# Performance work log

Measured on AMD Instinct MI355X. Metric: run time of the kernel, lower is better.

The kernel has to match this reference:

```python
import jax, jax.numpy as jnp
import numpy as np
import math

N = 20000          # real nodes (batch_size)
D = 256            # hidden_dim
H = 4              # num_heads
L = 3              # num_layers
E = 320000         # local edges
EXP_DEG = 4        # expander_degree
LN_EPS = 1e-5


def setup_inputs() -> dict:
    key = jax.random.key(0)
    ks = jax.random.split(key, 8)
    x = jax.random.normal(ks[0], (N, D), jnp.float32)
    rng = np.random.default_rng(0)
    edge_index = jnp.asarray(rng.integers(0, N, size=(2, E)), dtype=jnp.int32)
    # Expander: EXP_DEG//2 random permutations on N+1 nodes (incl. virtual node),
    # each contributing edges in both directions -> degree-EXP_DEG regular graph.
    n = N + 1
    perms = [rng.permutation(n) for _ in range(EXP_DEG // 2)]
    src = np.concatenate([np.arange(n) for _ in perms] + perms)
    dst = np.concatenate(perms + [np.arange(n) for _ in perms])
    exp_edge_index = jnp.asarray(np.stack([src, dst]), dtype=jnp.int32)
    s_in = 1.0 / math.sqrt(D)
    s_ffn = 1.0 / math.sqrt(4 * D)
    def w(k, shape, s):
        return jax.random.normal(k, shape, jnp.float32) * s
    params = {
        'Wqkv_loc': w(ks[1], (L, D, 3 * D), s_in), 'bqkv_loc': jnp.zeros((L, 3 * D), jnp.float32),
        'Wo_loc':   w(ks[2], (L, D, D), s_in),     'bo_loc':   jnp.zeros((L, D), jnp.float32),
        'Wqkv_exp': w(ks[3], (L, D, 3 * D), s_in), 'bqkv_exp': jnp.zeros((L, 3 * D), jnp.float32),
        'Wo_exp':   w(ks[4], (L, D, D), s_in),     'bo_exp':   jnp.zeros((L, D), jnp.float32),
        'ln_g': jnp.ones((L, D), jnp.float32),     'ln_b': jnp.zeros((L, D), jnp.float32),
        'W1': w(ks[5], (L, D, 4 * D), s_in),       'b1': jnp.zeros((L, 4 * D), jnp.float32),
        'W2': w(ks[6], (L, 4 * D, D), s_ffn),      'b2': jnp.zeros((L, D), jnp.float32),
    }
    return {'x': x, 'edge_index': edge_index, 'exp_edge_index': exp_edge_index, **params}


def _attention(h, src, dst, Wqkv, bqkv, Wo, bo):
    # Sparse multi-head attention over (src -> dst) edges with segment softmax per dst.
    n, d = h.shape
    dh = d // H
    qkv = (h @ Wqkv + bqkv).reshape(n, 3, H, dh)
    q, k, v = qkv[:, 0], qkv[:, 1], qkv[:, 2]            # [n, H, dh]
    score = (q[dst] * k[src]).sum(-1) / jnp.sqrt(jnp.float32(dh))  # [e, H]
    m = jax.ops.segment_max(score, dst, num_segments=n)  # [n, H]
    ex = jnp.exp(score - m[dst])
    denom = jax.ops.segment_sum(ex, dst, num_segments=n)
    alpha = ex / (denom[dst] + 1e-16)
    out = jax.ops.segment_sum(alpha[:, :, None] * v[src], dst, num_segments=n)  # [n, H, dh]
    return out.reshape(n, d) @ Wo + bo


def _layer_norm(x, g, b):
    mu = x.mean(-1, keepdims=True)
    var = ((x - mu) ** 2).mean(-1, keepdims=True)
    return (x - mu) * jax.lax.rsqrt(var + LN_EPS) * g + b


def reference(x, edge_index, exp_edge_index, Wqkv_loc, bqkv_loc, Wo_loc, bo_loc,
              Wqkv_exp, bqkv_exp, Wo_exp, bo_exp, ln_g, ln_b, W1, b1, W2, b2):
    n0 = x.shape[0]
    # VirtualNode transform: append one zero-feature node connected to/from all nodes.
    h = jnp.concatenate([x, jnp.zeros((1, x.shape[1]), x.dtype)], axis=0)
    ar = jnp.arange(n0, dtype=edge_index.dtype)
    vn = jnp.full((n0,), n0, dtype=edge_index.dtype)
    src = jnp.concatenate([edge_index[0], ar, vn])
    dst = jnp.concatenate([edge_index[1], vn, ar])
    esrc, edst = exp_edge_index[0], exp_edge_index[1]
    for l in range(L):  # fixed small number of structurally distinct layers
        res = h
        loc = _attention(h, src, dst, Wqkv_loc[l], bqkv_loc[l], Wo_loc[l], bo_loc[l])
        exp = _attention(h, esrc, edst, Wqkv_exp[l], bqkv_exp[l], Wo_exp[l], bo_exp[l])
        h = _layer_norm(res + loc + exp, ln_g[l], ln_b[l])
        h = h + (jax.nn.gelu(h @ W1[l] + b1[l], approximate=False) @ W2[l] + b2[l])
    return h[:n0]
```

## Files before the change

kernel.cpp:

```cpp
#include <hip/hip_runtime.h>
#include <stdint.h>

#define NREAL   20000
#define NNODES  20001
#define VN      20000
#define E_EDGES 320000
#define NEXP    80004
#define MPAD    20096
#define NVNW    320

typedef unsigned short u16;
typedef unsigned int   u32;
typedef __bf16 bf16x8 __attribute__((ext_vector_type(8)));
typedef float  f32x4  __attribute__((ext_vector_type(4)));

__device__ __host__ __forceinline__ size_t fmoff(int row, int col, int LD) {
    return (size_t)(row >> 4) * ((size_t)LD * 16) + (size_t)((col >> 3) * 128)
         + (size_t)((row & 15) * 8) + (size_t)(col & 7);
}

__device__ __forceinline__ float bf2f(u16 v) {
    union { u32 u; float f; } x; x.u = ((u32)v) << 16; return x.f;
}
__device__ __forceinline__ u16 f2bf(float f) {
    union { float f; u32 u; } x; x.f = f;
    u32 r = (x.u + 0x7fffu + ((x.u >> 16) & 1u)) >> 16;
    return (u16)r;
}
__device__ __forceinline__ float4 cvt4(ushort4 u) {
    return make_float4(bf2f(u.x), bf2f(u.y), bf2f(u.z), bf2f(u.w));
}
__device__ __forceinline__ float4 ld4bf(const u16* p) { return cvt4(*(const ushort4*)p); }


__global__ void hinit_kernel(const float* __restrict__ x, float* __restrict__ h,
                             u16* __restrict__ hb) {
    int idx = blockIdx.x * 256 + threadIdx.x;
    if (idx >= NNODES * 64) return;
    int row = idx >> 6, c0 = (idx & 63) * 4;
    float4 v = make_float4(0.f, 0.f, 0.f, 0.f);
    if (row < NREAL) v = *(const float4*)(x + (size_t)row * 256 + c0);
    *(float4*)(h + (size_t)row * 256 + c0) = v;
    ushort4 o;
    o.x = f2bf(v.x); o.y = f2bf(v.y); o.z = f2bf(v.z); o.w = f2bf(v.w);
    *(ushort4*)(hb + fmoff(row, c0, 256)) = o;
}

__global__ void init_kernel(int* cnt, int* fill, int* ecnt,
                            const float* __restrict__ bl, const float* __restrict__ be,
                            float* __restrict__ bcat,
                            const float* __restrict__ bol, const float* __restrict__ boe,
                            float* __restrict__ bsum) {
    int i = blockIdx.x * 256 + threadIdx.x;
    if (i < NREAL) { cnt[i] = 0; fill[i] = 0; }
    if (i < NNODES) ecnt[i] = 0;
    if (i < 3 * 1536) {
        int l = i / 1536, c = i - l * 1536;
        bcat[i] = (c < 768) ? bl[l * 768 + c] : be[l * 768 + c - 768];
    }
    if (i < 3 * 256) bsum[i] = bol[i] + boe[i];
}

__global__ void csr_count_kernel(const int* __restrict__ ei, int* __restrict__ cnt) {
    int e = blockIdx.x * 256 + threadIdx.x;
    if (e < E_EDGES) atomicAdd(&cnt[ei[E_EDGES + e]], 1);
}

__global__ void csr_scan_kernel(const int* __restrict__ cnt, int* __restrict__ indptr) {
    __shared__ int ssum[256];
    int t = threadIdx.x;
    int c0 = t * 79;
    int s = 0;
    for (int j = 0; j < 79; j++) {
        int i = c0 + j;
        if (i < NREAL) s += cnt[i];
    }
    ssum[t] = s;
    __syncthreads();
    for (int d2 = 1; d2 < 256; d2 <<= 1) {
        int v = (t >= d2) ? ssum[t - d2] : 0;
        __syncthreads();
        ssum[t] += v;
        __syncthreads();
    }
    int run = (t == 0) ? 0 : ssum[t - 1];
    for (int j = 0; j < 79; j++) {
        int i = c0 + j;
        if (i < NREAL) { indptr[i] = run; run += cnt[i]; }
    }
    if (t == 255) indptr[NREAL] = run;
}

__global__ void csr_scatter_kernel(const int* __restrict__ ei, const int* __restrict__ indptr,
                                   int* __restrict__ fill, int* __restrict__ srcs) {
    int e = blockIdx.x * 256 + threadIdx.x;
    if (e < E_EDGES) {
        int d = ei[E_EDGES + e];
        int pos = indptr[d] + atomicAdd(&fill[d], 1);
        srcs[pos] = ei[e];
    }
}

__global__ void exp_scatter_kernel(const int* __restrict__ eei, int* __restrict__ ecnt,
                                   int* __restrict__ esrcs) {
    int e = blockIdx.x * 256 + threadIdx.x;
    if (e < NEXP) {
        int d = eei[NEXP + e];
        int pos = atomicAdd(&ecnt[d], 1);
        esrcs[d * 4 + pos] = eei[e];
    }
}

__global__ void wconv_all_kernel(const float* __restrict__ WqkvL, const float* __restrict__ WqkvE,
                                 const float* __restrict__ WoL, const float* __restrict__ WoE,
                                 const float* __restrict__ W1, const float* __restrict__ W2,
                                 u16* __restrict__ out) {
    int i = blockIdx.x * 256 + threadIdx.x;
    if (i >= 3 * 1048576) return;
    int l = i / 1048576, r = i - l * 1048576;
    if (r >= 393216 && r < 524288) {
        int r2 = r - 393216;
        int k = r2 >> 8, n = r2 & 255;
        float v = (k < 256) ? WoL[(size_t)l * 65536 + k * 256 + n]
                            : WoE[(size_t)l * 65536 + (k - 256) * 256 + n];
        out[(size_t)l * 1048576 + 393216 + fmoff(n, k, 512)] = f2bf(v);
        return;
    }
    const float* src; int K, N; int base;
    if (r < 196608)      { src = WqkvL; K = 256;  N = 768;  base = 0; }
    else if (r < 393216) { src = WqkvE; K = 256;  N = 768;  base = 196608; }
    else if (r < 786432) { src = W1;    K = 256;  N = 1024; base = 524288; }
    else                 { src = W2;    K = 1024; N = 256;  base = 786432; }
    int r2 = r - base;
    int k = r2 / N, n = r2 - k * N;
    out[(size_t)l * 1048576 + base + fmoff(n, k, K)] = f2bf(src[(size_t)l * K * N + r2]);
}

template <int EPI>
__global__ __launch_bounds__(256) void gemm_bn(
    const u16* __restrict__ A, const u16* __restrict__ Bt, const float* __restrict__ bias,
    u16* Cb, u16* Q0, u16* KV0, u16* Q1, u16* KV1, int M, int Nout, int nbn) {
    __shared__ u16 lB[128 * 256];
    const int lin = blockIdx.x;
    const int xcd = lin & 7, rest = lin >> 3;
    const int nt = rest % nbn, mc = xcd + 8 * (rest / nbn);
    const int tn = nt * 128;
    const int tid = threadIdx.x;
    const int w = tid >> 6, lane = tid & 63;
    const int lm = lane & 15, q = lane >> 4;

    {
        const u16* bsrc = Bt + (size_t)(tn >> 4) * 4096;
#pragma unroll
        for (int r = 0; r < 16; r++) {
            int o = (r * 256 + tid) * 8;
            *(bf16x8*)&lB[o] = *(const bf16x8*)&bsrc[o];
        }
    }
    __syncthreads();

    f32x4 acc[2][8];
#pragma unroll
    for (int a = 0; a < 2; a++)
#pragma unroll
        for (int b = 0; b < 8; b++) acc[a][b] = (f32x4)0.0f;

    const int lbo = q * 128 + lm * 8;
    const int maxp = MPAD / 16 - 1;

    bf16x8 aS[3][2], bS[2][8];
#pragma unroll
    for (int s = 0; s < 2; s++) {
        int p0 = (mc * 4) * 8 + w * 2;
#pragma unroll
        for (int f = 0; f < 2; f++) {
            int p = p0 + f; if (p > maxp) p = maxp;
            aS[s][f] = *(const bf16x8*)(A + (size_t)p * 4096 + s * 512 + lbo);
        }
#pragma unroll
        for (int n = 0; n < 8; n++)
            bS[s][n] = *(const bf16x8*)&lB[n * 4096 + s * 512 + lbo];
    }

#pragma unroll
    for (int t = 0; t < 32; t++) {
        const int mt = t >> 3, kk = t & 7;
        if (t + 2 < 32) {
            const int t2 = t + 2, mt2 = t2 >> 3, kk2 = t2 & 7;
            int p0 = (mc * 4 + mt2) * 8 + w * 2;
#pragma unroll
            for (int f = 0; f < 2; f++) {
                int p = p0 + f; if (p > maxp) p = maxp;
                aS[t2 % 3][f] = *(const bf16x8*)(A + (size_t)p * 4096 + kk2 * 512 + lbo);
            }
        }
        if (t >= 1 && t + 1 < 32) {
            const int kk1 = (t + 1) & 7;
#pragma unroll
            for (int n = 0; n < 8; n++)
                bS[(t + 1) & 1][n] = *(const bf16x8*)&lB[n * 4096 + kk1 * 512 + lbo];
        }
#pragma unroll
        for (int mi = 0; mi < 2; mi++)
#pragma unroll
            for (int ni = 0; ni < 8; ni++)
                acc[mi][ni] = __builtin_amdgcn_mfma_f32_16x16x32_bf16(
                    bS[t & 1][ni], aS[t % 3][mi], acc[mi][ni], 0, 0, 0);

        if (kk == 7) {
            const int tmg = (mc * 4 + mt) * 128;
#pragma unroll
            for (int mi = 0; mi < 2; mi++) {
                int grow = tmg + w * 32 + mi * 16 + lm;
                if (grow < M) {
#pragma unroll
                    for (int ni = 0; ni < 8; ni++) {
                        int gcol = tn + ni * 16 + q * 4;
                        float4 b4 = *(const float4*)(bias + gcol);
                        float v0 = acc[mi][ni][0] + b4.x;
                        float v1 = acc[mi][ni][1] + b4.y;
                        float v2 = acc[mi][ni][2] + b4.z;
                        float v3 = acc[mi][ni][3] + b4.w;
                        if constexpr (EPI == 6) {
                            ushort4 o;
                            o.x = f2bf(v0); o.y = f2bf(v1); o.z = f2bf(v2); o.w = f2bf(v3);
                            u16* dst;
                            if (gcol < 256)       dst = Q0  + (size_t)grow * 256 + gcol;
                            else if (gcol < 768)  dst = KV0 + (size_t)grow * 512 + (gcol - 256);
                            else if (gcol < 1024) dst = Q1  + (size_t)grow * 256 + (gcol - 768);
                            else                  dst = KV1 + (size_t)grow * 512 + (gcol - 1024);
                            *(ushort4*)dst = o;
                        } else {
                            float g0, g1, g2, g3;
                            {
                                float u = 0.7978845608f * (v0 + 0.044715f * v0 * v0 * v0);
                                g0 = 0.5f * v0 * (2.0f - 2.0f / (__expf(2.0f * u) + 1.0f));
                            }
                            {
                                float u = 0.7978845608f * (v1 + 0.044715f * v1 * v1 * v1);
                                g1 = 0.5f * v1 * (2.0f - 2.0f / (__expf(2.0f * u) + 1.0f));
                            }
                            {
                                float u = 0.7978845608f * (v2 + 0.044715f * v2 * v2 * v2);
                                g2 = 0.5f * v2 * (2.0f - 2.0f / (__expf(2.0f * u) + 1.0f));
                            }
                            {
                                float u = 0.7978845608f * (v3 + 0.044715f * v3 * v3 * v3);
                                g3 = 0.5f * v3 * (2.0f - 2.0f / (__expf(2.0f * u) + 1.0f));
                            }
                            ushort4 o;
                            o.x = f2bf(g0); o.y = f2bf(g1); o.z = f2bf(g2); o.w = f2bf(g3);
                            *(ushort4*)(Cb + fmoff(grow, gcol, Nout)) = o;
                        }
                    }
                }
#pragma unroll
                for (int ni = 0; ni < 8; ni++) acc[mi][ni] = (f32x4)0.0f;
            }
        }
    }
}

template <int EPI, int K, int MT>
__global__ __launch_bounds__(256) void gemm_fm(
    const u16* __restrict__ A, const u16* __restrict__ Bt, const float* __restrict__ bias,
    u16* Cb, float* Cf, const float* resid, int M, int Nout, int nby) {
    constexpr int MFR = MT / 32;
    constexpr int NK = K / 32;
    const int lin = blockIdx.x;
    const int xcd = lin & 7, sub = lin >> 3;
    const int mtile = xcd + 8 * (sub / nby);
    const int ntile = sub - (sub / nby) * nby;
    const int tm = mtile * MT, tn = ntile * 128;
    if (tm >= M) return;

    const int tid = threadIdx.x;
    const int w = tid >> 6, lane = tid & 63;
    const int lm = lane & 15, q = lane >> 4;
    const int mo = (w >> 1) * (MT / 2), no = (w & 1) * 64;

    f32x4 acc[MFR][4];
#pragma unroll
    for (int a = 0; a < MFR; a++)
#pragma unroll
        for (int b = 0; b < 4; b++) acc[a][b] = (f32x4)0.0f;

    const u16* apf[MFR];
    const u16* bpf[4];
#pragma unroll
    for (int t = 0; t < MFR; t++) {
        int p = (tm + mo) / 16 + t;
        apf[t] = A + (size_t)p * (16 * K) + q * 128 + lm * 8;
    }
#pragma unroll
    for (int n = 0; n < 4; n++) {
        int c = (tn + no) / 16 + n;
        bpf[n] = Bt + (size_t)c * (16 * K) + q * 128 + lm * 8;
    }

    bf16x8 sA[3][MFR], sB[3][4];
#pragma unroll
    for (int s = 0; s < 2 && s < NK; s++) {
#pragma unroll
        for (int t = 0; t < MFR; t++) sA[s][t] = *(const bf16x8*)(apf[t] + s * 512);
#pragma unroll
        for (int n = 0; n < 4; n++) sB[s][n] = *(const bf16x8*)(bpf[n] + s * 512);
    }
#pragma unroll
    for (int i = 0; i < NK; i++) {
        const int cu = i % 3, pf = (i + 2) % 3;
        if (i + 2 < NK) {
#pragma unroll
            for (int t = 0; t < MFR; t++) sA[pf][t] = *(const bf16x8*)(apf[t] + (i + 2) * 512);
#pragma unroll
            for (int n = 0; n < 4; n++) sB[pf][n] = *(const bf16x8*)(bpf[n] + (i + 2) * 512);
        }
#pragma unroll
        for (int mi = 0; mi < MFR; mi++)
#pragma unroll
            for (int ni = 0; ni < 4; ni++)
                acc[mi][ni] = __builtin_amdgcn_mfma_f32_16x16x32_bf16(
                    sB[cu][ni], sA[cu][mi], acc[mi][ni], 0, 0, 0);
    }

    float4 b4[4];
#pragma unroll
    for (int ni = 0; ni < 4; ni++)
        b4[ni] = *(const float4*)(bias + tn + no + ni * 16 + q * 4);

#pragma unroll
    for (int mi = 0; mi < MFR; mi++) {
        int grow = tm + mo + mi * 16 + lm;
        if constexpr (EPI == 4) { if (grow >= NREAL) continue; }
        else                    { if (grow >= M) continue; }
#pragma unroll
        for (int ni = 0; ni < 4; ni++) {
            int gcol = tn + no + ni * 16 + q * 4;
            float v0 = acc[mi][ni][0] + b4[ni].x;
            float v1 = acc[mi][ni][1] + b4[ni].y;
            float v2 = acc[mi][ni][2] + b4[ni].z;
            float v3 = acc[mi][ni][3] + b4[ni].w;
            size_t idx = (size_t)grow * Nout + gcol;
            if constexpr (EPI == 1) {
                *(float4*)(Cf + idx) = make_float4(v0, v1, v2, v3);
            } else if constexpr (EPI == 3) {
                float4 rv = *(const float4*)(resid + idx);
                float o0 = rv.x + v0, o1 = rv.y + v1, o2 = rv.z + v2, o3 = rv.w + v3;
                *(float4*)(Cf + idx) = make_float4(o0, o1, o2, o3);
                ushort4 o;
                o.x = f2bf(o0); o.y = f2bf(o1); o.z = f2bf(o2); o.w = f2bf(o3);
                *(ushort4*)(Cb + fmoff(grow, gcol, Nout)) = o;
            } else {
                float4 rv = *(const float4*)(resid + idx);
                *(float4*)(Cf + idx) = make_float4(rv.x + v0, rv.y + v1, rv.z + v2, rv.w + v3);
            }
        }
    }
}

__global__ void vn_online_kernel(const u16* __restrict__ qb, const u16* __restrict__ kv,
                                 float* __restrict__ part) {
    int lane = threadIdx.x & 63;
    int h = lane >> 4;
    int off = (h << 6) + (lane & 15) * 4;
    float4 qv = ld4bf(qb + (size_t)VN * 256 + off);
    int wv = (int)((blockIdx.x * (size_t)blockDim.x + threadIdx.x) >> 6);
    float m = -1e30f, l = 0.0f;
    float ax = 0, ay = 0, az = 0, aw = 0;
    for (int i = wv; i < NREAL; i += NVNW) {
        const u16* p = kv + (size_t)i * 512 + off;
        float4 k4 = ld4bf(p);
        float4 v4 = ld4bf(p + 256);
        float s = qv.x * k4.x + qv.y * k4.y + qv.z * k4.z + qv.w * k4.w;
        s += __shfl_xor(s, 1); s += __shfl_xor(s, 2);
        s += __shfl_xor(s, 4); s += __shfl_xor(s, 8);
        float sc = s * 0.125f;
        float mn = fmaxf(m, sc);
        float fold = __expf(m - mn);
        float ee = __expf(sc - mn);
        ax = ax * fold + v4.x * ee;
        ay = ay * fold + v4.y * ee;
        az = az * fold + v4.z * ee;
        aw = aw * fold + v4.w * ee;
        l = l * fold + ee;
        m = mn;
    }
    float* pp = part + (size_t)wv * 264;
    if ((lane & 15) == 0) { pp[h] = m; pp[4 + h] = l; }
    *(float4*)(pp + 8 + off) = make_float4(ax, ay, az, aw);
}

__global__ void vn_merge_kernel(const float* __restrict__ part, u16* __restrict__ acat) {
    __shared__ float sm[4][64][6];
    int w = threadIdx.x >> 6, lane = threadIdx.x & 63;
    int h = lane >> 4;
    int off = (h << 6) + (lane & 15) * 4;
    float M = -1e30f, L = 0.0f;
    float ax = 0, ay = 0, az = 0, aw = 0;
    for (int p = w * 80; p < w * 80 + 80; p++) {
        const float* pp = part + (size_t)p * 264;
        float pm = pp[h], pl = pp[4 + h];
        float4 nm = *(const float4*)(pp + 8 + off);
        float Mn = fmaxf(M, pm);
        float s0 = __expf(M - Mn);
        float s1 = __expf(pm - Mn);
        ax = ax * s0 + nm.x * s1;
        ay = ay * s0 + nm.y * s1;
        az = az * s0 + nm.z * s1;
        aw = aw * s0 + nm.w * s1;
        L = L * s0 + pl * s1;
        M = Mn;
    }
    sm[w][lane][0] = M; sm[w][lane][1] = L;
    sm[w][lane][2] = ax; sm[w][lane][3] = ay;
    sm[w][lane][4] = az; sm[w][lane][5] = aw;
    __syncthreads();
    if (w == 0) {
        float M2 = -1e30f, L2 = 0.0f;
        float bx = 0, by = 0, bz = 0, bw = 0;
#pragma unroll
        for (int p = 0; p < 4; p++) {
            float pm = sm[p][lane][0], pl = sm[p][lane][1];
            float Mn = fmaxf(M2, pm);
            float s0 = __expf(M2 - Mn);
            float s1 = __expf(pm - Mn);
            bx = bx * s0 + sm[p][lane][2] * s1;
            by = by * s0 + sm[p][lane][3] * s1;
            bz = bz * s0 + sm[p][lane][4] * s1;
            bw = bw * s0 + sm[p][lane][5] * s1;
            L2 = L2 * s0 + pl * s1;
            M2 = Mn;
        }
        float inv = 1.0f / (L2 + 1e-16f);
        ushort4 o;
        o.x = f2bf(bx * inv); o.y = f2bf(by * inv);
        o.z = f2bf(bz * inv); o.w = f2bf(bw * inv);
        *(ushort4*)(acat + fmoff(VN, off, 512)) = o;
    }
}

__global__ void attn_fused_kernel(const u16* __restrict__ qb_loc, const u16* __restrict__ kv_loc,
                                  const u16* __restrict__ qb_exp, const u16* __restrict__ kv_exp,
                                  const int* __restrict__ indptr, const int* __restrict__ srcs,
                                  const int* __restrict__ esrcs,
                                  u16* __restrict__ acat) {
    int gw = (int)((blockIdx.x * (size_t)blockDim.x + threadIdx.x) >> 6);
    int lane = threadIdx.x & 63;
    int off = ((lane >> 4) << 6) + (lane & 15) * 4;

    const u16 *qb, *kv;
    const int* sl;
    int node, beg, deg, tot, cbase;
    if (gw < NREAL) {
        node = gw; qb = qb_loc; kv = kv_loc; sl = srcs; cbase = 0;
        beg = indptr[node]; deg = indptr[node + 1] - beg; tot = deg + 1;
    } else if (gw < NREAL + NNODES) {
        node = gw - NREAL;
        qb = qb_exp; kv = kv_exp; sl = esrcs; cbase = 256;
        beg = node * 4; deg = 4; tot = 4;
    } else {
        return;
    }

    float4 qv = ld4bf(qb + (size_t)node * 256 + off);
    float m = -1e30f, l = 0.0f;
    float ax = 0, ay = 0, az = 0, aw = 0;

    if (tot <= 4) {
        ushort4 kraw[4], vraw[4];
#pragma unroll
        for (int j = 0; j < 4; j++) {
            int s = (j < deg) ? sl[beg + j] : VN;
            const u16* p = kv + (size_t)s * 512 + off;
            kraw[j] = *(const ushort4*)p;
            vraw[j] = *(const ushort4*)(p + 256);
        }
        float sc[4];
#pragma unroll
        for (int j = 0; j < 4; j++) {
            float4 k4 = cvt4(kraw[j]);
            float p = qv.x * k4.x + qv.y * k4.y + qv.z * k4.z + qv.w * k4.w;
            p += __shfl_xor(p, 1); p += __shfl_xor(p, 2);
            p += __shfl_xor(p, 4); p += __shfl_xor(p, 8);
            sc[j] = (j < tot) ? p * 0.125f : -1e30f;
        }
        float mn = fmaxf(fmaxf(sc[0], sc[1]), fmaxf(sc[2], sc[3]));
#pragma unroll
        for (int j = 0; j < 4; j++) {
            float ee = __expf(sc[j] - mn);
            float4 v4 = cvt4(vraw[j]);
            ax += v4.x * ee; ay += v4.y * ee; az += v4.z * ee; aw += v4.w * ee;
            l += ee;
        }
        m = mn;
    } else {
        for (int e0 = 0; e0 < tot; e0 += 8) {
            ushort4 kraw[8], vraw[8];
#pragma unroll
            for (int j = 0; j < 8; j++) {
                int e = e0 + j;
                int s = (e < deg) ? sl[beg + e] : VN;
                const u16* p = kv + (size_t)s * 512 + off;
                kraw[j] = *(const ushort4*)p;
                vraw[j] = *(const ushort4*)(p + 256);
            }
            float sc[8];
#pragma unroll
            for (int j = 0; j < 8; j++) {
                float4 k4 = cvt4(kraw[j]);
                float p = qv.x * k4.x + qv.y * k4.y + qv.z * k4.z + qv.w * k4.w;
                p += __shfl_xor(p, 1); p += __shfl_xor(p, 2);
                p += __shfl_xor(p, 4); p += __shfl_xor(p, 8);
                sc[j] = (e0 + j < tot) ? p * 0.125f : -1e30f;
            }
            float cmax = fmaxf(fmaxf(fmaxf(sc[0], sc[1]), fmaxf(sc[2], sc[3])),
                               fmaxf(fmaxf(sc[4], sc[5]), fmaxf(sc[6], sc[7])));
            float mn = fmaxf(m, cmax);
            float fold = __expf(m - mn);
            ax *= fold; ay *= fold; az *= fold; aw *= fold; l *= fold;
#pragma unroll
            for (int j = 0; j < 8; j++) {
                float ee = __expf(sc[j] - mn);
                float4 v4 = cvt4(vraw[j]);
                ax += v4.x * ee; ay += v4.y * ee; az += v4.z * ee; aw += v4.w * ee;
                l += ee;
            }
            m = mn;
        }
    }
    float inv = 1.0f / (l + 1e-16f);
    ushort4 o;
    o.x = f2bf(ax * inv); o.y = f2bf(ay * inv);
    o.z = f2bf(az * inv); o.w = f2bf(aw * inv);
    *(ushort4*)(acat + fmoff(node, cbase + off, 512)) = o;
}

__global__ void ln_kernel(const float* hin, const float* __restrict__ asum,
                          const float* __restrict__ g, const float* __restrict__ b,
                          float* hout, u16* __restrict__ hb) {
    int row = blockIdx.x * 4 + (threadIdx.x >> 6);
    if (row >= NNODES) return;
    int lane = threadIdx.x & 63;
    size_t base = (size_t)row * 256 + lane * 4;
    float4 xv = *(const float4*)(hin + base);
    float4 av = *(const float4*)(asum + base);
    xv.x += av.x; xv.y += av.y; xv.z += av.z; xv.w += av.w;
    float s = xv.x + xv.y + xv.z + xv.w;
#pragma unroll
    for (int o = 1; o < 64; o <<= 1) s += __shfl_xor(s, o);
    float mu = s * (1.0f / 256.0f);
    float dx = xv.x - mu, dy = xv.y - mu, dz = xv.z - mu, dw = xv.w - mu;
    float ss = dx * dx + dy * dy + dz * dz + dw * dw;
#pragma unroll
    for (int o = 1; o < 64; o <<= 1) ss += __shfl_xor(ss, o);
    float var = ss * (1.0f / 256.0f);
    float inv = 1.0f / sqrtf(var + 1e-5f);
    float4 gv = *(const float4*)(g + lane * 4);
    float4 bv = *(const float4*)(b + lane * 4);
    float4 y;
    y.x = dx * inv * gv.x + bv.x;
    y.y = dy * inv * gv.y + bv.y;
    y.z = dz * inv * gv.z + bv.z;
    y.w = dw * inv * gv.w + bv.w;
    *(float4*)(hout + base) = y;
    ushort4 o4;
    o4.x = f2bf(y.x); o4.y = f2bf(y.y); o4.z = f2bf(y.z); o4.w = f2bf(y.w);
    *(ushort4*)(hb + fmoff(row, lane * 4, 256)) = o4;
}


extern "C" void kernel_launch(void* const* d_in, const int* in_sizes, int n_in,
                              void* d_out, int out_size, void* d_ws, size_t ws_size,
                              hipStream_t stream) {
    (void)in_sizes; (void)n_in; (void)out_size; (void)ws_size;
    const float* x        = (const float*)d_in[0];
    const int*   ei       = (const int*)d_in[1];
    const int*   eei      = (const int*)d_in[2];
    const float* Wqkv_loc = (const float*)d_in[3];
    const float* bqkv_loc = (const float*)d_in[4];
    const float* Wo_loc   = (const float*)d_in[5];
    const float* bo_loc   = (const float*)d_in[6];
    const float* Wqkv_exp = (const float*)d_in[7];
    const float* bqkv_exp = (const float*)d_in[8];
    const float* Wo_exp   = (const float*)d_in[9];
    const float* bo_exp   = (const float*)d_in[10];
    const float* ln_g     = (const float*)d_in[11];
    const float* ln_b     = (const float*)d_in[12];
    const float* W1       = (const float*)d_in[13];
    const float* b1       = (const float*)d_in[14];
    const float* W2       = (const float*)d_in[15];
    const float* b2       = (const float*)d_in[16];

    char* wsp = (char*)d_ws;
    size_t off = 0;
    auto carve = [&](size_t bytes) -> void* {
        void* p = wsp + off;
        off += (bytes + 255) & ~(size_t)255;
        return p;
    };
    float* h_f    = (float*)carve((size_t)NNODES * 256 * 4);
    u16*   h_b    = (u16*)carve((size_t)MPAD * 256 * 2);
    u16*   qb_loc = (u16*)carve((size_t)NNODES * 256 * 2);
    u16*   kv_loc = (u16*)carve((size_t)NNODES * 512 * 2);
    u16*   qb_exp = (u16*)carve((size_t)NNODES * 256 * 2);
    u16*   kv_exp = (u16*)carve((size_t)NNODES * 512 * 2);
    u16*   acat   = (u16*)carve((size_t)MPAD * 512 * 2);
    float* asum   = (float*)carve((size_t)NNODES * 256 * 4);
    u16*   wbf    = (u16*)carve((size_t)3 * 1048576 * 2);
    float* bcat   = (float*)carve((size_t)3 * 1536 * 4);
    float* bsum   = (float*)carve((size_t)3 * 256 * 4);
    int*   cnt    = (int*)carve((size_t)NREAL * 4);
    int*   indptr = (int*)carve((size_t)(NREAL + 1) * 4);
    int*   fill   = (int*)carve((size_t)NREAL * 4);
    int*   srcs   = (int*)carve((size_t)E_EDGES * 4);
    int*   ecnt   = (int*)carve((size_t)NNODES * 4);
    int*   esrcs  = (int*)carve((size_t)NNODES * 4 * 4);
    float* part   = (float*)carve((size_t)NVNW * 264 * 4);
    u16*   mid    = qb_loc;

    hinit_kernel<<<(NNODES * 64 + 255) / 256, 256, 0, stream>>>(x, h_f, h_b);
    init_kernel<<<(NNODES + 255) / 256, 256, 0, stream>>>(
        cnt, fill, ecnt, bqkv_loc, bqkv_exp, bcat, bo_loc, bo_exp, bsum);
    csr_count_kernel<<<(E_EDGES + 255) / 256, 256, 0, stream>>>(ei, cnt);
    csr_scan_kernel<<<1, 256, 0, stream>>>(cnt, indptr);
    csr_scatter_kernel<<<(E_EDGES + 255) / 256, 256, 0, stream>>>(ei, indptr, fill, srcs);
    exp_scatter_kernel<<<(NEXP + 255) / 256, 256, 0, stream>>>(eei, ecnt, esrcs);
    wconv_all_kernel<<<(3 * 1048576 + 255) / 256, 256, 0, stream>>>(
        Wqkv_loc, Wqkv_exp, Wo_loc, Wo_exp, W1, W2, wbf);

    const int NBM64 = 320;

    for (int l = 0; l < 3; l++) {
        const u16* wqkvC = wbf + (size_t)l * 1048576 + 0;
        const u16* wocat = wbf + (size_t)l * 1048576 + 393216;
        const u16* w1T   = wbf + (size_t)l * 1048576 + 524288;
        const u16* w2T   = wbf + (size_t)l * 1048576 + 786432;

        gemm_bn<6><<<480, 256, 0, stream>>>(
            h_b, wqkvC, bcat + l * 1536, nullptr,
            qb_loc, kv_loc, qb_exp, kv_exp, NNODES, 1536, 12);

        vn_online_kernel<<<NVNW / 4, 256, 0, stream>>>(qb_loc, kv_loc, part);
        vn_merge_kernel<<<1, 256, 0, stream>>>(part, acat);

        attn_fused_kernel<<<10001, 256, 0, stream>>>(
            qb_loc, kv_loc, qb_exp, kv_exp, indptr, srcs, esrcs, acat);

        gemm_fm<1, 512, 64><<<NBM64 * 2, 256, 0, stream>>>(
            acat, wocat, bsum + l * 256, nullptr, asum, nullptr, NNODES, 256, 2);

        ln_kernel<<<(NNODES + 3) / 4, 256, 0, stream>>>(
            h_f, asum, ln_g + l * 256, ln_b + l * 256, h_f, h_b);

        gemm_bn<2><<<320, 256, 0, stream>>>(
            h_b, w1T, b1 + l * 1024, mid,
            nullptr, nullptr, nullptr, nullptr, NNODES, 1024, 8);
        if (l < 2) {
            gemm_fm<3, 1024, 64><<<NBM64 * 2, 256, 0, stream>>>(
                mid, w2T, b2 + l * 256, h_b, h_f, h_f, NNODES, 256, 2);
        } else {
            gemm_fm<4, 1024, 64><<<NBM64 * 2, 256, 0, stream>>>(
                mid, w2T, b2 + l * 256, nullptr, (float*)d_out, h_f, NNODES, 256, 2);
        }
    }
}
```

Before: 910.5 us.

## Interleave K/V per lane, fuse VN attention into edge kernel, prefetch gathers

The QKV GEMM epilogue now stores K and V interleaved, so each lane fetches its 4 K and 4 V values with a single 16-byte load instead of two 8-byte loads in both attention paths. The virtual-node online-softmax kernel is folded into the fused edge-attention kernel as extra leading warps, which removes one launch and lets that work overlap with the per-node attention. The high-degree path also double-buffers the gathers for the next 8 edges while computing the current chunk. The cost is more registers in the prefetch path, which may lower occupancy, and the VN warps are now scheduled alongside the edge warps.

```diff
diff --git a/kernel.cpp b/kernel.cpp
--- a/kernel.cpp
+++ b/kernel.cpp
@@ -13,6 +13,7 @@
 typedef unsigned int   u32;
 typedef __bf16 bf16x8 __attribute__((ext_vector_type(8)));
 typedef float  f32x4  __attribute__((ext_vector_type(4)));
+typedef u16    u16x8  __attribute__((ext_vector_type(8)));
 
 __device__ __host__ __forceinline__ size_t fmoff(int row, int col, int LD) {
     return (size_t)(row >> 4) * ((size_t)LD * 16) + (size_t)((col >> 3) * 128)
@@ -31,6 +32,12 @@
     return make_float4(bf2f(u.x), bf2f(u.y), bf2f(u.z), bf2f(u.w));
 }
 __device__ __forceinline__ float4 ld4bf(const u16* p) { return cvt4(*(const ushort4*)p); }
+__device__ __forceinline__ float4 cvtk8(u16x8 r) {
+    return make_float4(bf2f(r[0]), bf2f(r[1]), bf2f(r[2]), bf2f(r[3]));
+}
+__device__ __forceinline__ float4 cvtv8(u16x8 r) {
+    return make_float4(bf2f(r[4]), bf2f(r[5]), bf2f(r[6]), bf2f(r[7]));
+}
 
 
 __global__ void hinit_kernel(const float* __restrict__ x, float* __restrict__ h,
@@ -225,10 +232,17 @@
                             ushort4 o;
                             o.x = f2bf(v0); o.y = f2bf(v1); o.z = f2bf(v2); o.w = f2bf(v3);
                             u16* dst;
-                            if (gcol < 256)       dst = Q0  + (size_t)grow * 256 + gcol;
-                            else if (gcol < 768)  dst = KV0 + (size_t)grow * 512 + (gcol - 256);
-                            else if (gcol < 1024) dst = Q1  + (size_t)grow * 256 + (gcol - 768);
-                            else                  dst = KV1 + (size_t)grow * 512 + (gcol - 1024);
+                            if (gcol < 256) {
+                                dst = Q0 + (size_t)grow * 256 + gcol;
+                            } else if (gcol < 768) {
+                                int c = gcol - 256;
+                                dst = KV0 + (size_t)grow * 512 + ((c & 255) >> 2) * 8 + ((c >> 8) << 2);
+                            } else if (gcol < 1024) {
+                                dst = Q1 + (size_t)grow * 256 + (gcol - 768);
+                            } else {
+                                int c = gcol - 1024;
+                                dst = KV1 + (size_t)grow * 512 + ((c & 255) >> 2) * 8 + ((c >> 8) << 2);
+                            }
                             *(ushort4*)dst = o;
                         } else {
                             float g0, g1, g2, g3;
@@ -358,38 +372,6 @@
     }
 }
 
-__global__ void vn_online_kernel(const u16* __restrict__ qb, const u16* __restrict__ kv,
-                                 float* __restrict__ part) {
-    int lane = threadIdx.x & 63;
-    int h = lane >> 4;
-    int off = (h << 6) + (lane & 15) * 4;
-    float4 qv = ld4bf(qb + (size_t)VN * 256 + off);
-    int wv = (int)((blockIdx.x * (size_t)blockDim.x + threadIdx.x) >> 6);
-    float m = -1e30f, l = 0.0f;
-    float ax = 0, ay = 0, az = 0, aw = 0;
-    for (int i = wv; i < NREAL; i += NVNW) {
-        const u16* p = kv + (size_t)i * 512 + off;
-        float4 k4 = ld4bf(p);
-        float4 v4 = ld4bf(p + 256);
-        float s = qv.x * k4.x + qv.y * k4.y + qv.z * k4.z + qv.w * k4.w;
-        s += __shfl_xor(s, 1); s += __shfl_xor(s, 2);
-        s += __shfl_xor(s, 4); s += __shfl_xor(s, 8);
-        float sc = s * 0.125f;
-        float mn = fmaxf(m, sc);
-        float fold = __expf(m - mn);
-        float ee = __expf(sc - mn);
-        ax = ax * fold + v4.x * ee;
-        ay = ay * fold + v4.y * ee;
-        az = az * fold + v4.z * ee;
-        aw = aw * fold + v4.w * ee;
-        l = l * fold + ee;
-        m = mn;
-    }
-    float* pp = part + (size_t)wv * 264;
-    if ((lane & 15) == 0) { pp[h] = m; pp[4 + h] = l; }
-    *(float4*)(pp + 8 + off) = make_float4(ax, ay, az, aw);
-}
-
 __global__ void vn_merge_kernel(const float* __restrict__ part, u16* __restrict__ acat) {
     __shared__ float sm[4][64][6];
     int w = threadIdx.x >> 6, lane = threadIdx.x & 63;
@@ -443,10 +425,43 @@
                                   const u16* __restrict__ qb_exp, const u16* __restrict__ kv_exp,
                                   const int* __restrict__ indptr, const int* __restrict__ srcs,
                                   const int* __restrict__ esrcs,
-                                  u16* __restrict__ acat) {
-    int gw = (int)((blockIdx.x * (size_t)blockDim.x + threadIdx.x) >> 6);
+                                  u16* __restrict__ acat, float* __restrict__ part) {
+    int gw0 = (int)((blockIdx.x * (size_t)blockDim.x + threadIdx.x) >> 6);
+    int gw = __builtin_amdgcn_readfirstlane(gw0);
     int lane = threadIdx.x & 63;
-    int off = ((lane >> 4) << 6) + (lane & 15) * 4;
+    int h = lane >> 4;
+    int off = (h << 6) + (lane & 15) * 4;
+    int coff = (off >> 2) * 8;
+
+    if (gw < NVNW) {
+        int wv = gw;
+        float4 qv = ld4bf(qb_loc + (size_t)VN * 256 + off);
+        float m = -1e30f, l = 0.0f;
+        float ax = 0, ay = 0, az = 0, aw = 0;
+        for (int i = wv; i < NREAL; i += NVNW) {
+            u16x8 r = *(const u16x8*)(kv_loc + (size_t)i * 512 + coff);
+            float4 k4 = cvtk8(r);
+            float4 v4 = cvtv8(r);
+            float s = qv.x * k4.x + qv.y * k4.y + qv.z * k4.z + qv.w * k4.w;
+            s += __shfl_xor(s, 1); s += __shfl_xor(s, 2);
+            s += __shfl_xor(s, 4); s += __shfl_xor(s, 8);
+            float sc = s * 0.125f;
+            float mn = fmaxf(m, sc);
+            float fold = __expf(m - mn);
+            float ee = __expf(sc - mn);
+            ax = ax * fold + v4.x * ee;
+            ay = ay * fold + v4.y * ee;
+            az = az * fold + v4.z * ee;
+            aw = aw * fold + v4.w * ee;
+            l = l * fold + ee;
+            m = mn;
+        }
+        float* pp = part + (size_t)wv * 264;
+        if ((lane & 15) == 0) { pp[h] = m; pp[4 + h] = l; }
+        *(float4*)(pp + 8 + off) = make_float4(ax, ay, az, aw);
+        return;
+    }
+    gw -= NVNW;
 
     const u16 *qb, *kv;
     const int* sl;
@@ -467,18 +482,16 @@
     float ax = 0, ay = 0, az = 0, aw = 0;
 
     if (tot <= 4) {
-        ushort4 kraw[4], vraw[4];
+        u16x8 raw[4];
 #pragma unroll
         for (int j = 0; j < 4; j++) {
             int s = (j < deg) ? sl[beg + j] : VN;
-            const u16* p = kv + (size_t)s * 512 + off;
-            kraw[j] = *(const ushort4*)p;
-            vraw[j] = *(const ushort4*)(p + 256);
+            raw[j] = *(const u16x8*)(kv + (size_t)s * 512 + coff);
         }
         float sc[4];
 #pragma unroll
         for (int j = 0; j < 4; j++) {
-            float4 k4 = cvt4(kraw[j]);
+            float4 k4 = cvtk8(raw[j]);
             float p = qv.x * k4.x + qv.y * k4.y + qv.z * k4.z + qv.w * k4.w;
             p += __shfl_xor(p, 1); p += __shfl_xor(p, 2);
             p += __shfl_xor(p, 4); p += __shfl_xor(p, 8);
@@ -488,26 +501,34 @@
 #pragma unroll
         for (int j = 0; j < 4; j++) {
             float ee = __expf(sc[j] - mn);
-            float4 v4 = cvt4(vraw[j]);
+            float4 v4 = cvtv8(raw[j]);
             ax += v4.x * ee; ay += v4.y * ee; az += v4.z * ee; aw += v4.w * ee;
             l += ee;
         }
         m = mn;
     } else {
-        for (int e0 = 0; e0 < tot; e0 += 8) {
-            ushort4 kraw[8], vraw[8];
+        const int nch = (tot + 7) >> 3;
+        u16x8 rA[8], rB[8];
+#pragma unroll
+        for (int j = 0; j < 8; j++) {
+            int s = (j < deg) ? sl[beg + j] : VN;
+            rA[j] = *(const u16x8*)(kv + (size_t)s * 512 + coff);
+        }
+        for (int c = 0; c < nch; c++) {
+            if (c + 1 < nch) {
+                const int e0n = (c + 1) * 8;
+#pragma unroll
+                for (int j = 0; j < 8; j++) {
+                    int e = e0n + j;
+                    int s = (e < deg) ? sl[beg + e] : VN;
+                    rB[j] = *(const u16x8*)(kv + (size_t)s * 512 + coff);
+                }
+            }
+            const int e0 = c * 8;
+            float sc[8];
 #pragma unroll
             for (int j = 0; j < 8; j++) {
-                int e = e0 + j;
-                int s = (e < deg) ? sl[beg + e] : VN;
-                const u16* p = kv + (size_t)s * 512 + off;
-                kraw[j] = *(const ushort4*)p;
-                vraw[j] = *(const ushort4*)(p + 256);
-            }
-            float sc[8];
-#pragma unroll
-            for (int j = 0; j < 8; j++) {
-                float4 k4 = cvt4(kraw[j]);
+                float4 k4 = cvtk8(rA[j]);
                 float p = qv.x * k4.x + qv.y * k4.y + qv.z * k4.z + qv.w * k4.w;
                 p += __shfl_xor(p, 1); p += __shfl_xor(p, 2);
                 p += __shfl_xor(p, 4); p += __shfl_xor(p, 8);
@@ -521,11 +542,13 @@
 #pragma unroll
             for (int j = 0; j < 8; j++) {
                 float ee = __expf(sc[j] - mn);
-                float4 v4 = cvt4(vraw[j]);
+                float4 v4 = cvtv8(rA[j]);
                 ax += v4.x * ee; ay += v4.y * ee; az += v4.z * ee; aw += v4.w * ee;
                 l += ee;
             }
             m = mn;
+#pragma unroll
+            for (int j = 0; j < 8; j++) rA[j] = rB[j];
         }
     }
     float inv = 1.0f / (l + 1e-16f);
@@ -629,6 +652,7 @@
         Wqkv_loc, Wqkv_exp, Wo_loc, Wo_exp, W1, W2, wbf);
 
     const int NBM64 = 320;
+    const int ATTN_BLOCKS = (NVNW + NREAL + NNODES + 3) / 4;
 
     for (int l = 0; l < 3; l++) {
         const u16* wqkvC = wbf + (size_t)l * 1048576 + 0;
@@ -640,11 +664,9 @@
             h_b, wqkvC, bcat + l * 1536, nullptr,
             qb_loc, kv_loc, qb_exp, kv_exp, NNODES, 1536, 12);
 
-        vn_online_kernel<<<NVNW / 4, 256, 0, stream>>>(qb_loc, kv_loc, part);
+        attn_fused_kernel<<<ATTN_BLOCKS, 256, 0, stream>>>(
+            qb_loc, kv_loc, qb_exp, kv_exp, indptr, srcs, esrcs, acat, part);
         vn_merge_kernel<<<1, 256, 0, stream>>>(part, acat);
-
-        attn_fused_kernel<<<10001, 256, 0, stream>>>(
-            qb_loc, kv_loc, qb_exp, kv_exp, indptr, srcs, esrcs, acat);
 
         gemm_fm<1, 512, 64><<<NBM64 * 2, 256, 0, stream>>>(
             acat, wocat, bsum + l * 256, nullptr, asum, nullptr, NNODES, 256, 2);
```

After: 1.093 ms. +20.0%, slower.
